# Performance work log

Hardware: AMD Instinct MI355X
Metric: run time of the kernel (lower is better)

The kernel has to match this reference:

```python
import jax, jax.numpy as jnp
import numpy as np


def setup_inputs() -> dict:
    key = jax.random.key(0)
    kq, kk, kv = jax.random.split(key, 3)
    B, L, H, D = 2, 4096, 8, 64
    queries = jax.random.normal(kq, (B, L, H, D), dtype=jnp.float32)
    keys = jax.random.normal(kk, (B, L, H, D), dtype=jnp.float32)
    values = jax.random.normal(kv, (B, L, H, D), dtype=jnp.float32)
    return {"queries": queries, "keys": keys, "values": values}


def reference(queries, keys, values):
    # queries/keys/values: [B, L, H, D]
    d_model = queries.shape[-1]
    scale = 1.0 / jnp.sqrt(jnp.asarray(d_model, dtype=queries.dtype))
    # scores: [B, H, Lq, Lk]
    scores = jnp.einsum('blhd,bshd->bhls', queries, keys)
    # dropout is identity in eval mode / for deterministic reference
    A = jax.nn.softmax(scale * scores, axis=-1)
    # output: [B, Lq, H, D]
    V = jnp.einsum('bhls,bshd->blhd', A, values)
    return V
```

## Files before the change

kernel.cpp:

```cpp
#include <hip/hip_runtime.h>

#define Bn 2
#define Ln 4096
#define Hn 8
#define Dn 64
#define NMEGA 32
#define BH_STRIDE 262144

typedef float    f32x4 __attribute__((ext_vector_type(4)));
typedef _Float16 f16x4 __attribute__((ext_vector_type(4)));
typedef _Float16 f16x8 __attribute__((ext_vector_type(8)));

static __device__ __forceinline__ void gld16(const void* g, void* l){
    __builtin_amdgcn_global_load_lds(
        (const __attribute__((address_space(1))) unsigned int*)g,
        (__attribute__((address_space(3))) unsigned int*)l, 16, 0, 0);
}

__global__ __launch_bounds__(256)
void kvprep(const float* __restrict__ Kg, const float* __restrict__ Vg,
            _Float16* __restrict__ kp, _Float16* __restrict__ vp){
    __shared__ float tile[64*65];
    const int t = blockIdx.x, bh = blockIdx.y, b = bh>>3, h = bh&7;
    const int tid = threadIdx.x;
#pragma unroll
    for(int i=0;i<2;++i){
        int u = tid + i*256;
        int row = u>>3, blk = (u&7) ^ (row&7);
        const float* src = Kg + (((size_t)b*Ln + t*64 + row)*Hn + h)*Dn + blk*8;
        float4 a = *(const float4*)src;
        float4 c = *(const float4*)(src + 4);
        f16x8 o;
        o[0]=(_Float16)a.x; o[1]=(_Float16)a.y; o[2]=(_Float16)a.z; o[3]=(_Float16)a.w;
        o[4]=(_Float16)c.x; o[5]=(_Float16)c.y; o[6]=(_Float16)c.z; o[7]=(_Float16)c.w;
        *(f16x8*)(kp + (size_t)bh*BH_STRIDE + t*4096 + (size_t)u*8) = o;
    }
#pragma unroll
    for(int i=0;i<4;++i){
        int idx = tid + i*256;
        int k = idx >> 4, d4 = (idx & 15)*4;
        float4 v = *(const float4*)(Vg + (((size_t)b*Ln + t*64 + k)*Hn + h)*Dn + d4);
        tile[k*65 + d4+0]=v.x; tile[k*65+d4+1]=v.y;
        tile[k*65 + d4+2]=v.z; tile[k*65+d4+3]=v.w;
    }
    __syncthreads();
#pragma unroll
    for(int i=0;i<2;++i){
        int u = tid + i*256;
        int d = u>>3, s = u&7;
        int x = s ^ (d&7);
        int lg = x>>1, gh = x&1;
        f16x8 o;
#pragma unroll
        for(int j2=0;j2<8;++j2){
            int g = gh*2 + (j2>>2), j = j2&3;
            int k = g*16 + lg*4 + j;
            o[j2] = (_Float16)tile[k*65 + d];
        }
        *(f16x8*)(vp + (size_t)bh*BH_STRIDE + t*4096 + (size_t)u*8) = o;
    }
}

__global__ __launch_bounds__(256,2)
void attn_fwd(const float* __restrict__ Qg, float* __restrict__ Og,
              const _Float16* __restrict__ kp, const _Float16* __restrict__ vp){
    __shared__ __align__(16) _Float16 sK[2][8192];
    __shared__ __align__(16) _Float16 sV[2][8192];

    const int tid  = threadIdx.x;
    const int lane = tid & 63, wv = tid >> 6;
    const int qh = wv & 1, kh2 = wv >> 1;
    const int ln15 = lane & 15, lg = lane >> 4, ln7 = ln15 & 7;
    const int bh = blockIdx.x, b = bh>>3, h = bh&7;
    const int q0 = blockIdx.y*128 + qh*64;

    const float c = 0.125f * 1.4426950408889634f;

    f16x8 qf[4][2];
#pragma unroll
    for(int qt=0;qt<4;++qt){
        const float* qrow = Qg + (((size_t)b*Ln + q0 + qt*16 + ln15)*Hn + h)*Dn;
#pragma unroll
        for(int ch=0;ch<2;++ch){
            const float* p4 = qrow + ch*32 + lg*8;
            float4 x = *(const float4*)p4;
            float4 y = *(const float4*)(p4+4);
            f16x8 f;
            f[0]=(_Float16)(x.x*c); f[1]=(_Float16)(x.y*c);
            f[2]=(_Float16)(x.z*c); f[3]=(_Float16)(x.w*c);
            f[4]=(_Float16)(y.x*c); f[5]=(_Float16)(y.y*c);
            f[6]=(_Float16)(y.z*c); f[7]=(_Float16)(y.w*c);
            qf[qt][ch]=f;
        }
    }

    f32x4 o[4][4];
    f32x4 lac[4];
#pragma unroll
    for(int qt=0;qt<4;++qt){
        lac[qt] = (f32x4){0.f,0.f,0.f,0.f};
#pragma unroll
        for(int dt=0;dt<4;++dt) o[qt][dt] = (f32x4){0.f,0.f,0.f,0.f};
    }

    const _Float16* kg = kp + (size_t)bh*BH_STRIDE;
    const _Float16* vg = vp + (size_t)bh*BH_STRIDE;

    const int half = kh2*8192;
    const int kb0 = half + ln15*128 + (((0+lg) ^ ln7) << 4);
    const int kb1 = half + ln15*128 + (((4+lg) ^ ln7) << 4);
    int vbofs[2];
#pragma unroll
    for(int gh=0; gh<2; ++gh)
        vbofs[gh] = half + ln15*128 + (((lg*2+gh) ^ ln7) << 4);

#pragma unroll
    for(int i=0;i<4;++i){
        int u = i*256 + tid;
        gld16(kg + (size_t)u*8, &sK[0][(size_t)u*8]);
        gld16(vg + (size_t)u*8, &sV[0][(size_t)u*8]);
    }

    for(int T=0; T<NMEGA; ++T){
        __syncthreads();
        const int cur = T & 1;
        if(T+1 < NMEGA){
            const int nxt = cur ^ 1;
            const _Float16* kgn = kg + (size_t)(T+1)*8192;
            const _Float16* vgn = vg + (size_t)(T+1)*8192;
#pragma unroll
            for(int i=0;i<4;++i){
                int u = i*256 + tid;
                gld16(kgn + (size_t)u*8, &sK[nxt][(size_t)u*8]);
                gld16(vgn + (size_t)u*8, &sV[nxt][(size_t)u*8]);
            }
        }

        f16x8 W[4][2];
#pragma unroll
        for(int dt=0;dt<4;++dt)
#pragma unroll
            for(int gh=0;gh<2;++gh)
                W[dt][gh] = *(const f16x8*)((const char*)&sV[cur][0] + dt*2048 + vbofs[gh]);

#pragma unroll
        for(int g=0; g<4; ++g){
            f16x8 kf0 = *(const f16x8*)((const char*)&sK[cur][0] + g*2048 + kb0);
            f16x8 kf1 = *(const f16x8*)((const char*)&sK[cur][0] + g*2048 + kb1);
#pragma unroll
            for(int qt=0;qt<4;++qt){
                f32x4 s = (f32x4){0.f,0.f,0.f,0.f};
                s = __builtin_amdgcn_mfma_f32_16x16x32_f16(kf0, qf[qt][0], s, 0,0,0);
                s = __builtin_amdgcn_mfma_f32_16x16x32_f16(kf1, qf[qt][1], s, 0,0,0);
                f32x4 p;
                p[0] = __builtin_amdgcn_exp2f(s[0]);
                p[1] = __builtin_amdgcn_exp2f(s[1]);
                p[2] = __builtin_amdgcn_exp2f(s[2]);
                p[3] = __builtin_amdgcn_exp2f(s[3]);
                lac[qt] += p;
                f16x4 pa;
                pa[0]=(_Float16)p[0]; pa[1]=(_Float16)p[1];
                pa[2]=(_Float16)p[2]; pa[3]=(_Float16)p[3];
#pragma unroll
                for(int dt=0;dt<4;++dt){
                    f16x8 Wd = W[dt][g>>1];
                    f16x4 vf = (g & 1)
                        ? __builtin_shufflevector(Wd, Wd, 4,5,6,7)
                        : __builtin_shufflevector(Wd, Wd, 0,1,2,3);
                    o[qt][dt] = __builtin_amdgcn_mfma_f32_16x16x16f16(pa, vf, o[qt][dt], 0,0,0);
                }
            }
        }
    }

    float lred[4];
#pragma unroll
    for(int qt=0;qt<4;++qt){
        float l = (lac[qt][0]+lac[qt][1]) + (lac[qt][2]+lac[qt][3]);
        l += __shfl_xor(l, 16, 64);
        l += __shfl_xor(l, 32, 64);
        lred[qt] = l;
    }

    __syncthreads();
    float* xo = (float*)&sK[0][0];
    float* xl = xo + 2*64*68;
    if(kh2){
#pragma unroll
        for(int qt=0;qt<4;++qt){
#pragma unroll
            for(int dt=0;dt<4;++dt)
#pragma unroll
                for(int r=0;r<4;++r)
                    xo[(qh*64 + qt*16 + lg*4 + r)*68 + dt*16 + ln15] = o[qt][dt][r];
            if(lg==0) xl[qh*64 + qt*16 + ln15] = lred[qt];
        }
    }
    __syncthreads();
    if(!kh2){
#pragma unroll
        for(int qt=0;qt<4;++qt){
            float lt = lred[qt] + xl[qh*64 + qt*16 + ln15];
            float inv = 1.0f/lt;
            float invr[4];
#pragma unroll
            for(int r=0;r<4;++r) invr[r] = __shfl(inv, lg*4 + r, 64);
            float* ob = Og + (((size_t)b*Ln + q0 + qt*16)*Hn + h)*Dn;
#pragma unroll
            for(int dt=0;dt<4;++dt)
#pragma unroll
                for(int r=0;r<4;++r){
                    float val = o[qt][dt][r]
                              + xo[(qh*64 + qt*16 + lg*4 + r)*68 + dt*16 + ln15];
                    ob[(size_t)(lg*4+r)*Hn*Dn + dt*16 + ln15] = val*invr[r];
                }
        }
    }
}

extern "C" void kernel_launch(void* const* d_in, const int* in_sizes, int n_in,
                              void* d_out, int out_size, void* d_ws, size_t ws_size,
                              hipStream_t stream) {
    const float* Q = (const float*)d_in[0];
    const float* K = (const float*)d_in[1];
    const float* V = (const float*)d_in[2];
    float* O = (float*)d_out;

    _Float16* kp = (_Float16*)d_ws;
    _Float16* vp = (_Float16*)((char*)d_ws + (8u<<20));

    kvprep<<<dim3(64, 16), dim3(256), 0, stream>>>(K, V, kp, vp);
    attn_fwd<<<dim3(16, 32), dim3(256), 0, stream>>>(Q, O, kp, vp);
}
```

Baseline: 169.4 us.

## Single-buffer V in LDS to cut shared memory and raise occupancy

V is now single-buffered in LDS. Each iteration loads the V fragments into registers and then hits an extra barrier before the prefetch of the next tile overwrites the buffer. This shrinks shared memory from 64KB to 48KB, and launch bounds are raised to 3 blocks per CU to get more waves resident. It also replaces the per-element fp16 casts of P with packed round-toward-zero conversions and reduces the row-sum accumulator to a scalar. The costs are an extra barrier per tile, possible register pressure under the tighter launch bound, and slightly different rounding of the probabilities.

```diff
diff --git a/kernel.cpp b/kernel.cpp
--- a/kernel.cpp
+++ b/kernel.cpp
@@ -8,6 +8,7 @@
 #define BH_STRIDE 262144
 
 typedef float    f32x4 __attribute__((ext_vector_type(4)));
+typedef __fp16   h16x2 __attribute__((ext_vector_type(2)));
 typedef _Float16 f16x4 __attribute__((ext_vector_type(4)));
 typedef _Float16 f16x8 __attribute__((ext_vector_type(8)));
 
@@ -61,11 +62,10 @@
     }
 }
 
-__global__ __launch_bounds__(256,2)
+__global__ __launch_bounds__(256,3)
 void attn_fwd(const float* __restrict__ Qg, float* __restrict__ Og,
               const _Float16* __restrict__ kp, const _Float16* __restrict__ vp){
-    __shared__ __align__(16) _Float16 sK[2][8192];
-    __shared__ __align__(16) _Float16 sV[2][8192];
+    __shared__ __align__(16) char sAll[49152];
 
     const int tid  = threadIdx.x;
     const int lane = tid & 63, wv = tid >> 6;
@@ -95,16 +95,17 @@
     }
 
     f32x4 o[4][4];
-    f32x4 lac[4];
+    float lac[4];
 #pragma unroll
     for(int qt=0;qt<4;++qt){
-        lac[qt] = (f32x4){0.f,0.f,0.f,0.f};
+        lac[qt] = 0.f;
 #pragma unroll
         for(int dt=0;dt<4;++dt) o[qt][dt] = (f32x4){0.f,0.f,0.f,0.f};
     }
 
     const _Float16* kg = kp + (size_t)bh*BH_STRIDE;
     const _Float16* vg = vp + (size_t)bh*BH_STRIDE;
+    char* const Vb = sAll + 32768;
 
     const int half = kh2*8192;
     const int kb0 = half + ln15*128 + (((0+lg) ^ ln7) << 4);
@@ -117,50 +118,54 @@
 #pragma unroll
     for(int i=0;i<4;++i){
         int u = i*256 + tid;
-        gld16(kg + (size_t)u*8, &sK[0][(size_t)u*8]);
-        gld16(vg + (size_t)u*8, &sV[0][(size_t)u*8]);
+        gld16(kg + (size_t)u*8, sAll + (size_t)u*16);
+        gld16(vg + (size_t)u*8, Vb   + (size_t)u*16);
     }
 
     for(int T=0; T<NMEGA; ++T){
         __syncthreads();
-        const int cur = T & 1;
+        const char* Kc = sAll + (T&1)*16384;
+
+        f16x8 W[4][2];
+#pragma unroll
+        for(int dt=0;dt<4;++dt)
+#pragma unroll
+            for(int gh=0;gh<2;++gh)
+                W[dt][gh] = *(const f16x8*)(Vb + dt*2048 + vbofs[gh]);
+
+        __syncthreads();
+
         if(T+1 < NMEGA){
-            const int nxt = cur ^ 1;
+            char* Kn = sAll + ((T+1)&1)*16384;
             const _Float16* kgn = kg + (size_t)(T+1)*8192;
             const _Float16* vgn = vg + (size_t)(T+1)*8192;
 #pragma unroll
             for(int i=0;i<4;++i){
                 int u = i*256 + tid;
-                gld16(kgn + (size_t)u*8, &sK[nxt][(size_t)u*8]);
-                gld16(vgn + (size_t)u*8, &sV[nxt][(size_t)u*8]);
+                gld16(kgn + (size_t)u*8, Kn + (size_t)u*16);
+                gld16(vgn + (size_t)u*8, Vb + (size_t)u*16);
             }
         }
 
-        f16x8 W[4][2];
-#pragma unroll
-        for(int dt=0;dt<4;++dt)
-#pragma unroll
-            for(int gh=0;gh<2;++gh)
-                W[dt][gh] = *(const f16x8*)((const char*)&sV[cur][0] + dt*2048 + vbofs[gh]);
-
 #pragma unroll
         for(int g=0; g<4; ++g){
-            f16x8 kf0 = *(const f16x8*)((const char*)&sK[cur][0] + g*2048 + kb0);
-            f16x8 kf1 = *(const f16x8*)((const char*)&sK[cur][0] + g*2048 + kb1);
+            f16x8 kf0 = *(const f16x8*)(Kc + g*2048 + kb0);
+            f16x8 kf1 = *(const f16x8*)(Kc + g*2048 + kb1);
 #pragma unroll
             for(int qt=0;qt<4;++qt){
                 f32x4 s = (f32x4){0.f,0.f,0.f,0.f};
                 s = __builtin_amdgcn_mfma_f32_16x16x32_f16(kf0, qf[qt][0], s, 0,0,0);
                 s = __builtin_amdgcn_mfma_f32_16x16x32_f16(kf1, qf[qt][1], s, 0,0,0);
-                f32x4 p;
-                p[0] = __builtin_amdgcn_exp2f(s[0]);
-                p[1] = __builtin_amdgcn_exp2f(s[1]);
-                p[2] = __builtin_amdgcn_exp2f(s[2]);
-                p[3] = __builtin_amdgcn_exp2f(s[3]);
-                lac[qt] += p;
+                float p0 = __builtin_amdgcn_exp2f(s[0]);
+                float p1 = __builtin_amdgcn_exp2f(s[1]);
+                float p2 = __builtin_amdgcn_exp2f(s[2]);
+                float p3 = __builtin_amdgcn_exp2f(s[3]);
+                lac[qt] += (p0+p1)+(p2+p3);
+                h16x2 c01 = __builtin_amdgcn_cvt_pkrtz(p0, p1);
+                h16x2 c23 = __builtin_amdgcn_cvt_pkrtz(p2, p3);
                 f16x4 pa;
-                pa[0]=(_Float16)p[0]; pa[1]=(_Float16)p[1];
-                pa[2]=(_Float16)p[2]; pa[3]=(_Float16)p[3];
+                pa[0]=(_Float16)c01[0]; pa[1]=(_Float16)c01[1];
+                pa[2]=(_Float16)c23[0]; pa[3]=(_Float16)c23[1];
 #pragma unroll
                 for(int dt=0;dt<4;++dt){
                     f16x8 Wd = W[dt][g>>1];
@@ -176,15 +181,15 @@
     float lred[4];
 #pragma unroll
     for(int qt=0;qt<4;++qt){
-        float l = (lac[qt][0]+lac[qt][1]) + (lac[qt][2]+lac[qt][3]);
+        float l = lac[qt];
         l += __shfl_xor(l, 16, 64);
         l += __shfl_xor(l, 32, 64);
         lred[qt] = l;
     }
 
     __syncthreads();
-    float* xo = (float*)&sK[0][0];
-    float* xl = xo + 2*64*68;
+    float* xo = (float*)sAll;
+    float* xl = xo + 128*68;
     if(kh2){
 #pragma unroll
         for(int qt=0;qt<4;++qt){
```

After: 349.3 us. 106% more time.
